# Optimization experiments

Hardware: AMD Instinct MI355X
Metric: run time of the kernel (lower is better)

The kernel has to match this reference:

```python
import jax, jax.numpy as jnp
import numpy as np

D_MODEL = 1024
D_STATE = 16
D_CONV = 3
EXPAND = 2
D_INNER = EXPAND * D_MODEL
BATCH = 1
SEQ = 2048


def _xavier(key, fan_in, fan_out, shape):
    lim = float(np.sqrt(6.0 / (fan_in + fan_out)))
    return jax.random.uniform(key, shape, jnp.float32, -lim, lim)


def setup_inputs() -> dict:
    key = jax.random.key(0)
    ks = jax.random.split(key, 8)
    return {
        "x": jax.random.normal(ks[0], (BATCH, SEQ, D_MODEL), jnp.float32),
        # torch Linear weight (out,in) stored transposed as (in,out) for x @ W
        "in_proj_w": _xavier(ks[1], D_MODEL, 2 * D_INNER, (D_MODEL, 2 * D_INNER)),
        "in_proj_b": jnp.zeros((2 * D_INNER,), jnp.float32),
        "conv_w": _xavier(ks[2], D_MODEL * D_CONV, D_INNER, (D_INNER, D_MODEL, D_CONV)),
        "conv_b": jax.random.normal(ks[3], (D_INNER,), jnp.float32) * 0.02,
        # A_log shifted negative so softplus(A_log) is tiny and the (unstable-by-construction)
        # recurrence with A_bar=exp(+A*dt)>1 stays finite over SEQ steps
        "A_log": jax.random.normal(ks[4], (D_INNER, D_STATE), jnp.float32) * 0.1 - 6.0,
        "D": jnp.ones((D_INNER,), jnp.float32),
        "x_proj_w": _xavier(ks[5], D_INNER, 2 * D_STATE, (D_INNER, 2 * D_STATE)),
        "x_proj_b": jnp.zeros((2 * D_STATE,), jnp.float32),
        "gate_w": _xavier(ks[6], D_INNER, D_INNER, (D_INNER, D_INNER)),
        "gate_b": jnp.zeros((D_INNER,), jnp.float32),
        "o_proj_w": _xavier(ks[7], D_INNER, D_MODEL, (D_INNER, D_MODEL)),
        "o_proj_b": jnp.zeros((D_MODEL,), jnp.float32),
    }


def _forward(x, in_proj_w, in_proj_b, conv_w, conv_b, A_log, D, x_proj_w, x_proj_b,
             gate_w, gate_b, o_proj_w, o_proj_b):
    B, S, _ = x.shape
    # causal depthful conv: torch pads both sides by d_conv-1 then truncates to S,
    # which equals left-pad-only by d_conv-1
    xc = jax.lax.conv_general_dilated(
        x.transpose(0, 2, 1), conv_w, (1,), [(D_CONV - 1, 0)],
        dimension_numbers=("NCH", "OIH", "NCH"))
    x_conv = xc.transpose(0, 2, 1) + conv_b            # (B,S,d_inner)

    xz = x @ in_proj_w + in_proj_b                      # (B,S,2*d_inner)
    z = xz[..., D_INNER:]                               # gate branch (x_inner unused)

    A = jax.nn.softplus(A_log)                          # (d_inner,d_state)
    bc = x_conv @ x_proj_w + x_proj_b                   # (B,S,2*d_state)
    Bm, Cm = bc[..., :D_STATE], bc[..., D_STATE:]
    dt = jax.nn.sigmoid(jnp.mean(x_conv, axis=-1, keepdims=True)) + 0.001  # (B,S,1)
    gate = jax.nn.sigmoid(x_conv @ gate_w + gate_b)
    u = x_conv * gate                                   # (B,S,d_inner)

    dtE = dt[..., None]                                 # (B,S,1,1)
    A_bar = jnp.exp(A[None, None] * dtE)                # (B,S,d_inner,d_state)
    B_bar = A_bar * Bm[:, :, None, :] * dtE             # (B,S,d_inner,d_state)

    def step(h, inp):
        ab, bb, ut, ct = inp                            # (B,di,ds),(B,di,ds),(B,di),(B,ds)
        h = ab * h + bb * ut[:, :, None]
        y = jnp.einsum("bds,bs->bd", h, ct) + D * ut
        return h, y

    h0 = jnp.zeros((B, D_INNER, D_STATE), x.dtype)
    _, ys = jax.lax.scan(
        step, h0,
        (A_bar.transpose(1, 0, 2, 3), B_bar.transpose(1, 0, 2, 3),
         u.transpose(1, 0, 2), Cm.transpose(1, 0, 2)))
    out = ys.transpose(1, 0, 2) * jax.nn.sigmoid(z)     # (B,S,d_inner)
    return out @ o_proj_w + o_proj_b                    # (B,S,d_model)


def reference(x, in_proj_w, in_proj_b, conv_w, conv_b, A_log, D, x_proj_w, x_proj_b,
              gate_w, gate_b, o_proj_w, o_proj_b):
    return _forward(x, in_proj_w, in_proj_b, conv_w, conv_b, A_log, D,
                    x_proj_w, x_proj_b, gate_w, gate_b, o_proj_w, o_proj_b)
```

## Files before the change

kernel.cpp:

```cpp
#include <hip/hip_runtime.h>
#include <hip/hip_bf16.h>
#include <math.h>

typedef __attribute__((ext_vector_type(8))) short short8;
typedef __attribute__((ext_vector_type(4))) float f32x4;

#define NCH 128
#define CT 16

__device__ __forceinline__ unsigned short f2bf(float f) {
  unsigned u = __builtin_bit_cast(unsigned, f);
  u += 0x7fffu + ((u >> 16) & 1u);
  return (unsigned short)(u >> 16);
}
__device__ __forceinline__ float bf2f(unsigned short u) {
  return __builtin_bit_cast(float, (unsigned)u << 16);
}
__device__ __forceinline__ float sigm(float x) { return 1.f / (1.f + __expf(-x)); }

__device__ __forceinline__ void stage16(const void* g, void* l) {
  __builtin_amdgcn_global_load_lds(
      (const __attribute__((address_space(1))) unsigned int*)(unsigned long long)g,
      (__attribute__((address_space(3))) unsigned int*)(unsigned)(unsigned long long)l,
      16, 0, 0);
}

__global__ void prep_xpad(const float* __restrict__ x, unsigned short* __restrict__ xb) {
  int idx = (blockIdx.x * 256 + threadIdx.x) * 4;
  if (idx >= 2050 * 1024) return;
  int row = idx >> 10, col = idx & 1023;
  float v0 = 0.f, v1 = 0.f, v2 = 0.f, v3 = 0.f;
  if (row >= 2) {
    const float4 v = *(const float4*)(x + (size_t)(row - 2) * 1024 + col);
    v0 = v.x; v1 = v.y; v2 = v.z; v3 = v.w;
  }
  unsigned long long pk = (unsigned long long)f2bf(v0)
      | ((unsigned long long)f2bf(v1) << 16)
      | ((unsigned long long)f2bf(v2) << 32)
      | ((unsigned long long)f2bf(v3) << 48);
  *(unsigned long long*)(xb + idx) = pk;
}

__global__ void prep_convw(const float* __restrict__ cw, unsigned short* __restrict__ cwt) {
  int idx = blockIdx.x * 256 + threadIdx.x;
  int d = idx >> 10, i = idx & 1023;
  const float* p = cw + (size_t)d * 3072 + (size_t)i * 3;
  unsigned short* q = cwt + (size_t)d * 3072 + i;
  q[0] = f2bf(p[0]);
  q[1024] = f2bf(p[1]);
  q[2048] = f2bf(p[2]);
}

__global__ void prep_cA(const float* __restrict__ A_log, float* __restrict__ cAb) {
  int i = blockIdx.x * 256 + threadIdx.x;
  cAb[i] = log1pf(__expf(A_log[i]));
}

__global__ void transpose_bf16(const float* __restrict__ W, int src_ld, int col_off,
                               unsigned short* __restrict__ Wt, int rowsI) {
  __shared__ float tile[32][33];
  int n0 = blockIdx.x * 32, i0 = blockIdx.y * 32;
  int tx = threadIdx.x & 31, ty = threadIdx.x >> 5;
#pragma unroll
  for (int rr = 0; rr < 32; rr += 8)
    tile[ty + rr][tx] = W[(size_t)(i0 + ty + rr) * src_ld + col_off + n0 + tx];
  __syncthreads();
#pragma unroll
  for (int rr = 0; rr < 32; rr += 8)
    Wt[(size_t)(n0 + ty + rr) * rowsI + i0 + tx] = f2bf(tile[tx][ty + rr]);
}

template <int MODE, int BM, int BN>
__global__ __launch_bounds__(256, 2) void gemm_t(
    const unsigned short* __restrict__ A, int lda,
    const unsigned short* __restrict__ Bt, int ldb, int K,
    const float* __restrict__ bias,
    float* __restrict__ outf, int ldo,
    unsigned short* __restrict__ outb,
    const unsigned short* __restrict__ mulsrc) {
  constexpr int MR = BM / 32;
  constexpr int NR = BN / 32;
  constexpr int IA = BM / 32;
  constexpr int IB = BN / 32;
  constexpr int L = IA + IB;
  __shared__ unsigned short As[3][BM * 64];
  __shared__ unsigned short Bs[3][BN * 64];

  const int tid = threadIdx.x;
  const int lane = tid & 63;
  const int w = tid >> 6;
  const int wr = w >> 1, wc = w & 1;
  const int bm = blockIdx.x, bn = blockIdx.y;

  f32x4 acc[MR][NR];
#pragma unroll
  for (int m = 0; m < MR; ++m)
#pragma unroll
    for (int n = 0; n < NR; ++n)
#pragma unroll
      for (int j = 0; j < 4; ++j) acc[m][n][j] = 0.f;

  const int srow = lane >> 3;
  const int sslot = (lane & 7) ^ srow;
  const unsigned short* Ab = A + (size_t)(bm * BM + srow) * lda + sslot * 8;
  const unsigned short* Bb = Bt + (size_t)(bn * BN + srow) * ldb + sslot * 8;

  const int r = lane & 15;
  const int g = lane >> 4;
  const int nk = K >> 6;

  auto stage = [&](int buf, int k0) {
#pragma unroll
    for (int i = 0; i < IA; ++i) {
      const int cb = w * IA + i;
      stage16(Ab + (size_t)(cb * 8) * lda + k0, &As[buf][cb * 512]);
    }
#pragma unroll
    for (int i = 0; i < IB; ++i) {
      const int cb = w * IB + i;
      stage16(Bb + (size_t)(cb * 8) * ldb + k0, &Bs[buf][cb * 512]);
    }
  };

  auto compute = [&](int buf) {
#pragma unroll
    for (int kk = 0; kk < 64; kk += 32) {
      const int sb = (kk >> 3) + g;
      short8 af[MR], bfr[NR];
#pragma unroll
      for (int m = 0; m < MR; ++m) {
        const int R = wr * (BM / 2) + m * 16 + r;
        af[m] = *(const short8*)&As[buf][R * 64 + ((sb ^ (R & 7)) << 3)];
      }
#pragma unroll
      for (int n = 0; n < NR; ++n) {
        const int R = wc * (BN / 2) + n * 16 + r;
        bfr[n] = *(const short8*)&Bs[buf][R * 64 + ((sb ^ (R & 7)) << 3)];
      }
#pragma unroll
      for (int m = 0; m < MR; ++m)
#pragma unroll
        for (int n = 0; n < NR; ++n)
          acc[m][n] = __builtin_amdgcn_mfma_f32_16x16x32_bf16(af[m], bfr[n], acc[m][n], 0, 0, 0);
    }
  };

  stage(0, 0);
  stage(1, 64);
  int cur = 0, nxt = 2;
  for (int kt = 0; kt < nk; ++kt) {
    if (kt + 2 < nk) {
      stage(nxt, (kt + 2) * 64);
      asm volatile("s_waitcnt vmcnt(%c0)" ::"i"(2 * L) : "memory");
    } else if (kt + 1 < nk) {
      asm volatile("s_waitcnt vmcnt(%c0)" ::"i"(L) : "memory");
    } else {
      asm volatile("s_waitcnt vmcnt(0)" ::: "memory");
    }
    __builtin_amdgcn_s_barrier();
    __builtin_amdgcn_sched_barrier(0);
    compute(cur);
    __builtin_amdgcn_s_barrier();
    cur = (cur == 2) ? 0 : cur + 1;
    nxt = (nxt == 2) ? 0 : nxt + 1;
  }

  const int cc = lane & 15;
  const int cr = g * 4;
#pragma unroll
  for (int m = 0; m < MR; ++m) {
#pragma unroll
    for (int n = 0; n < NR; ++n) {
      const int col = bn * BN + wc * (BN / 2) + n * 16 + cc;
      const float bv = bias[col];
#pragma unroll
      for (int j = 0; j < 4; ++j) {
        const int row = bm * BM + wr * (BM / 2) + m * 16 + cr + j;
        const size_t o = (size_t)row * ldo + col;
        float v = acc[m][n][j] + bv;
        if (MODE == 0) { outb[o] = f2bf(v); }
        else if (MODE == 1) { outf[o] = v; }
        else { outb[o] = f2bf(bf2f(mulsrc[o]) * sigm(v)); }
      }
    }
  }
}

#define RB 4
__global__ __launch_bounds__(256) void bcdt(const unsigned short* __restrict__ xcb,
                                            const float* __restrict__ xpw,
                                            const float* __restrict__ xpb,
                                            float* __restrict__ Bc, float* __restrict__ Cc,
                                            float* __restrict__ dt) {
  int s0 = blockIdx.x * RB;
  __shared__ float row[RB][2048];
  __shared__ float pj[RB][8][32];
  const int lane = threadIdx.x & 63, wv = threadIdx.x >> 6;
  for (int i = threadIdx.x; i < RB * 256; i += 256) {
    int ri = i >> 8, c8 = i & 255;
    short8 v = *(const short8*)&xcb[(size_t)(s0 + ri) * 2048 + c8 * 8];
#pragma unroll
    for (int j = 0; j < 8; ++j) row[ri][c8 * 8 + j] = bf2f((unsigned short)v[j]);
  }
  __syncthreads();
  {
    float l = 0.f;
    for (int i = lane; i < 2048; i += 64) l += row[wv][i];
#pragma unroll
    for (int off = 32; off > 0; off >>= 1) l += __shfl_down(l, off);
    if (lane == 0) dt[s0 + wv] = sigm(l * (1.f / 2048.f)) + 0.001f;
  }
  const int j = threadIdx.x & 31, seg = threadIdx.x >> 5;
  float acc[RB] = {0.f, 0.f, 0.f, 0.f};
  const int kbase = seg * 256;
  for (int k = 0; k < 256; ++k) {
    float wv2 = xpw[(size_t)(kbase + k) * 32 + j];
#pragma unroll
    for (int ri = 0; ri < RB; ++ri) acc[ri] += row[ri][kbase + k] * wv2;
  }
#pragma unroll
  for (int ri = 0; ri < RB; ++ri) pj[ri][seg][j] = acc[ri];
  __syncthreads();
  if (threadIdx.x < 32 * RB) {
    int ri = threadIdx.x >> 5, jj = threadIdx.x & 31;
    float v = xpb[jj];
#pragma unroll
    for (int q = 0; q < 8; ++q) v += pj[ri][q][jj];
    if (jj < 16) Bc[(size_t)(s0 + ri) * 16 + jj] = v;
    else Cc[(size_t)(s0 + ri) * 16 + jj - 16] = v;
  }
}

__global__ void dtcum(const float* __restrict__ dt, float* __restrict__ T,
                      float* __restrict__ S) {
  int c = threadIdx.x;
  if (c < NCH) {
    float acc = 0.f;
#pragma unroll
    for (int t = 0; t < CT; ++t) {
      acc += dt[c * CT + t];
      T[c * CT + t] = acc;
    }
    S[c] = acc;
  }
}

__global__ __launch_bounds__(256) void scan_local(const float* __restrict__ cAb,
                                                  const float* __restrict__ dt,
                                                  const float* __restrict__ Bc,
                                                  const float* __restrict__ Cc,
                                                  const unsigned short* __restrict__ u,
                                                  const float* __restrict__ Dp,
                                                  unsigned short* __restrict__ yloc,
                                                  float* __restrict__ Hend) {
  const int d0 = blockIdx.x * 256;
  const int d = d0 + threadIdx.x;
  const int c = blockIdx.y;
  __shared__ float sU[CT][256];
  __shared__ float sB[CT][16], sC[CT][16], sdt[CT];
  for (int i = threadIdx.x; i < CT * 32; i += 256) {
    int t = i >> 5, c8 = i & 31;
    short8 v = *(const short8*)&u[(size_t)(c * CT + t) * 2048 + d0 + c8 * 8];
#pragma unroll
    for (int j = 0; j < 8; ++j) sU[t][c8 * 8 + j] = bf2f((unsigned short)v[j]);
  }
  for (int i = threadIdx.x; i < CT * 16; i += 256) {
    sB[i >> 4][i & 15] = Bc[(size_t)c * CT * 16 + i];
    sC[i >> 4][i & 15] = Cc[(size_t)c * CT * 16 + i];
  }
  if (threadIdx.x < CT) sdt[threadIdx.x] = dt[c * CT + threadIdx.x];
  __syncthreads();
  float cA[16], h[16];
#pragma unroll
  for (int n = 0; n < 16; ++n) {
    cA[n] = cAb[(size_t)d * 16 + n];
    h[n] = 0.f;
  }
  const float Dv = Dp[d];
  for (int t = 0; t < CT; ++t) {
    const float dtv = sdt[t];
    const float uv = sU[t][threadIdx.x];
    const float du = dtv * uv;
    float y = Dv * uv;
#pragma unroll
    for (int n = 0; n < 16; ++n) {
      float ab = __expf(cA[n] * dtv);
      h[n] = ab * (h[n] + sB[t][n] * du);
      y += h[n] * sC[t][n];
    }
    yloc[(size_t)(c * CT + t) * 2048 + d] = f2bf(y);
  }
#pragma unroll
  for (int n = 0; n < 16; ++n) Hend[(size_t)c * 32768 + (size_t)d * 16 + n] = h[n];
}

__global__ __launch_bounds__(64) void scan_carry(const float* __restrict__ cAb,
                                                 const float* __restrict__ S,
                                                 float* H) {
  const int g = blockIdx.x * 64 + threadIdx.x;
  const float cA = cAb[g];
  __shared__ float sS[NCH];
  for (int i = threadIdx.x; i < NCH; i += 64) sS[i] = S[i];
  __syncthreads();
  float h = 0.f;
  for (int cb = 0; cb < NCH; cb += 16) {
    float hl[16];
#pragma unroll
    for (int i = 0; i < 16; ++i) hl[i] = H[(size_t)(cb + i) * 32768 + g];
#pragma unroll
    for (int i = 0; i < 16; ++i) {
      H[(size_t)(cb + i) * 32768 + g] = h;
      h = __expf(cA * sS[cb + i]) * h + hl[i];
    }
  }
}

__global__ __launch_bounds__(256) void scan_final(const float* __restrict__ cAb,
                                                  const float* __restrict__ T,
                                                  const float* __restrict__ Cc,
                                                  const unsigned short* __restrict__ yloc,
                                                  const unsigned short* __restrict__ zpre,
                                                  const float* __restrict__ H,
                                                  unsigned short* __restrict__ ob) {
  const int d = blockIdx.x * 256 + threadIdx.x;
  const int c = blockIdx.y;
  __shared__ float sC[CT][16], sT[CT];
  for (int i = threadIdx.x; i < CT * 16; i += 256) sC[i >> 4][i & 15] = Cc[(size_t)c * CT * 16 + i];
  if (threadIdx.x < CT) sT[threadIdx.x] = T[c * CT + threadIdx.x];
  __syncthreads();
  float cA[16], h0[16];
#pragma unroll
  for (int n = 0; n < 16; ++n) {
    cA[n] = cAb[(size_t)d * 16 + n];
    h0[n] = H[(size_t)c * 32768 + (size_t)d * 16 + n];
  }
  for (int t = 0; t < CT; ++t) {
    const size_t idx = (size_t)(c * CT + t) * 2048 + d;
    const float Tt = sT[t];
    float y = bf2f(yloc[idx]);
#pragma unroll
    for (int n = 0; n < 16; ++n) y += sC[t][n] * __expf(cA[n] * Tt) * h0[n];
    ob[idx] = f2bf(y * sigm(bf2f(zpre[idx])));
  }
}

extern "C" void kernel_launch(void* const* d_in, const int* in_sizes, int n_in,
                              void* d_out, int out_size, void* d_ws, size_t ws_size,
                              hipStream_t stream) {
  (void)in_sizes; (void)n_in; (void)out_size; (void)ws_size;
  const float* x = (const float*)d_in[0];
  const float* in_proj_w = (const float*)d_in[1];
  const float* in_proj_b = (const float*)d_in[2];
  const float* conv_w = (const float*)d_in[3];
  const float* conv_b = (const float*)d_in[4];
  const float* A_log = (const float*)d_in[5];
  const float* Dp = (const float*)d_in[6];
  const float* x_proj_w = (const float*)d_in[7];
  const float* x_proj_b = (const float*)d_in[8];
  const float* gate_w = (const float*)d_in[9];
  const float* gate_b = (const float*)d_in[10];
  const float* o_proj_w = (const float*)d_in[11];
  const float* o_proj_b = (const float*)d_in[12];

  char* ws = (char*)d_ws;
  size_t off = 0;
  unsigned short* xb = (unsigned short*)(ws + off); off += (size_t)2050 * 1024 * 2;
  off = (off + 255) & ~(size_t)255;
  unsigned short* cwt = (unsigned short*)(ws + off); off += (size_t)2048 * 3072 * 2;
  unsigned short* wzt = (unsigned short*)(ws + off); off += (size_t)2048 * 1024 * 2;
  unsigned short* gwt = (unsigned short*)(ws + off); off += (size_t)2048 * 2048 * 2;
  unsigned short* owt = (unsigned short*)(ws + off); off += (size_t)1024 * 2048 * 2;
  unsigned short* xcb = (unsigned short*)(ws + off); off += (size_t)2048 * 2048 * 2;
  unsigned short* zpre_b = (unsigned short*)(ws + off); off += (size_t)2048 * 2048 * 2;
  unsigned short* uu_b = (unsigned short*)(ws + off); off += (size_t)2048 * 2048 * 2;
  unsigned short* yloc = (unsigned short*)(ws + off); off += (size_t)2048 * 2048 * 2;
  float* dtv = (float*)(ws + off); off += (size_t)2048 * 4;
  float* Bc = (float*)(ws + off); off += (size_t)2048 * 16 * 4;
  float* Cc = (float*)(ws + off); off += (size_t)2048 * 16 * 4;
  float* Tcum = (float*)(ws + off); off += (size_t)2048 * 4;
  float* Ssum = (float*)(ws + off); off += (size_t)NCH * 4;
  float* cAb = (float*)(ws + off); off += (size_t)32768 * 4;
  float* H = (float*)(ws + off); off += (size_t)NCH * 32768 * 4;
  unsigned short* ob = xcb;

  prep_xpad<<<2050, 256, 0, stream>>>(x, xb);
  prep_convw<<<8192, 256, 0, stream>>>(conv_w, cwt);
  prep_cA<<<128, 256, 0, stream>>>(A_log, cAb);
  transpose_bf16<<<dim3(64, 32), 256, 0, stream>>>(in_proj_w, 4096, 2048, wzt, 1024);
  transpose_bf16<<<dim3(64, 64), 256, 0, stream>>>(gate_w, 2048, 0, gwt, 2048);
  transpose_bf16<<<dim3(32, 64), 256, 0, stream>>>(o_proj_w, 1024, 0, owt, 2048);

  gemm_t<0, 128, 64><<<dim3(16, 32), 256, 0, stream>>>(xb, 1024, cwt, 3072, 3072, conv_b, nullptr, 2048, xcb, nullptr);
  gemm_t<0, 128, 64><<<dim3(16, 32), 256, 0, stream>>>(xb + 2 * 1024, 1024, wzt, 1024, 1024, in_proj_b + 2048, nullptr, 2048, zpre_b, nullptr);
  bcdt<<<512, 256, 0, stream>>>(xcb, x_proj_w, x_proj_b, Bc, Cc, dtv);
  dtcum<<<1, 128, 0, stream>>>(dtv, Tcum, Ssum);
  gemm_t<2, 128, 64><<<dim3(16, 32), 256, 0, stream>>>(xcb, 2048, gwt, 2048, 2048, gate_b, nullptr, 2048, uu_b, xcb);

  scan_local<<<dim3(8, NCH), 256, 0, stream>>>(cAb, dtv, Bc, Cc, uu_b, Dp, yloc, H);
  scan_carry<<<512, 64, 0, stream>>>(cAb, Ssum, H);
  scan_final<<<dim3(8, NCH), 256, 0, stream>>>(cAb, Tcum, Cc, yloc, zpre_b, H, ob);

  gemm_t<1, 64, 64><<<dim3(32, 16), 256, 0, stream>>>(ob, 2048, owt, 2048, 2048, o_proj_b, (float*)d_out, 1024, nullptr, nullptr);
}
```

Measured before the change: 178.9 us.

## Merge prep kernels, fuse conv and z GEMMs, fold dtcum into scans

Six preprocessing kernels are merged into one launch that dispatches on block index. The conv and z-projection GEMMs are merged into one launch using 128x128 tiles with double buffering, and the gate GEMM also moves to 128x128 tiles. The separate dtcum kernel is removed: chunk sums are computed inside scan_carry and prefix sums inside scan_final. The aim is fewer launches and less per-launch overhead, at the cost of fewer blocks per GEMM and a shallower prefetch pipeline.

```diff
diff --git a/kernel.cpp b/kernel.cpp
--- a/kernel.cpp
+++ b/kernel.cpp
@@ -25,41 +25,64 @@
       16, 0, 0);
 }
 
-__global__ void prep_xpad(const float* __restrict__ x, unsigned short* __restrict__ xb) {
-  int idx = (blockIdx.x * 256 + threadIdx.x) * 4;
-  if (idx >= 2050 * 1024) return;
-  int row = idx >> 10, col = idx & 1023;
-  float v0 = 0.f, v1 = 0.f, v2 = 0.f, v3 = 0.f;
-  if (row >= 2) {
-    const float4 v = *(const float4*)(x + (size_t)(row - 2) * 1024 + col);
-    v0 = v.x; v1 = v.y; v2 = v.z; v3 = v.w;
-  }
-  unsigned long long pk = (unsigned long long)f2bf(v0)
-      | ((unsigned long long)f2bf(v1) << 16)
-      | ((unsigned long long)f2bf(v2) << 32)
-      | ((unsigned long long)f2bf(v3) << 48);
-  *(unsigned long long*)(xb + idx) = pk;
-}
-
-__global__ void prep_convw(const float* __restrict__ cw, unsigned short* __restrict__ cwt) {
-  int idx = blockIdx.x * 256 + threadIdx.x;
-  int d = idx >> 10, i = idx & 1023;
-  const float* p = cw + (size_t)d * 3072 + (size_t)i * 3;
-  unsigned short* q = cwt + (size_t)d * 3072 + i;
-  q[0] = f2bf(p[0]);
-  q[1024] = f2bf(p[1]);
-  q[2048] = f2bf(p[2]);
-}
-
-__global__ void prep_cA(const float* __restrict__ A_log, float* __restrict__ cAb) {
-  int i = blockIdx.x * 256 + threadIdx.x;
-  cAb[i] = log1pf(__expf(A_log[i]));
-}
-
-__global__ void transpose_bf16(const float* __restrict__ W, int src_ld, int col_off,
-                               unsigned short* __restrict__ Wt, int rowsI) {
+__global__ __launch_bounds__(256) void prep_uber(
+    const float* __restrict__ x, const float* __restrict__ conv_w,
+    const float* __restrict__ A_log, const float* __restrict__ in_proj_w,
+    const float* __restrict__ gate_w, const float* __restrict__ o_proj_w,
+    unsigned short* __restrict__ xb, unsigned short* __restrict__ cwt,
+    float* __restrict__ cAb, unsigned short* __restrict__ wzt,
+    unsigned short* __restrict__ gwt, unsigned short* __restrict__ owt) {
   __shared__ float tile[32][33];
-  int n0 = blockIdx.x * 32, i0 = blockIdx.y * 32;
+  int bx = blockIdx.x;
+  if (bx < 2050) {
+    int idx = (bx * 256 + threadIdx.x) * 4;
+    if (idx >= 2050 * 1024) return;
+    int row = idx >> 10, col = idx & 1023;
+    float v0 = 0.f, v1 = 0.f, v2 = 0.f, v3 = 0.f;
+    if (row >= 2) {
+      const float4 v = *(const float4*)(x + (size_t)(row - 2) * 1024 + col);
+      v0 = v.x; v1 = v.y; v2 = v.z; v3 = v.w;
+    }
+    unsigned long long pk = (unsigned long long)f2bf(v0)
+        | ((unsigned long long)f2bf(v1) << 16)
+        | ((unsigned long long)f2bf(v2) << 32)
+        | ((unsigned long long)f2bf(v3) << 48);
+    *(unsigned long long*)(xb + idx) = pk;
+    return;
+  }
+  bx -= 2050;
+  if (bx < 8192) {
+    int idx = bx * 256 + threadIdx.x;
+    int d = idx >> 10, i = idx & 1023;
+    const float* p = conv_w + (size_t)d * 3072 + (size_t)i * 3;
+    unsigned short* q = cwt + (size_t)d * 3072 + i;
+    q[0] = f2bf(p[0]);
+    q[1024] = f2bf(p[1]);
+    q[2048] = f2bf(p[2]);
+    return;
+  }
+  bx -= 8192;
+  if (bx < 128) {
+    int i = bx * 256 + threadIdx.x;
+    cAb[i] = log1pf(__expf(A_log[i]));
+    return;
+  }
+  bx -= 128;
+  const float* W;
+  unsigned short* Wt;
+  int src_ld, col_off, rowsI, n0, i0;
+  if (bx < 2048) {
+    W = in_proj_w; Wt = wzt; src_ld = 4096; col_off = 2048; rowsI = 1024;
+    n0 = (bx & 63) * 32; i0 = (bx >> 6) * 32;
+  } else if (bx < 2048 + 4096) {
+    int b = bx - 2048;
+    W = gate_w; Wt = gwt; src_ld = 2048; col_off = 0; rowsI = 2048;
+    n0 = (b & 63) * 32; i0 = (b >> 6) * 32;
+  } else {
+    int b = bx - 2048 - 4096;
+    W = o_proj_w; Wt = owt; src_ld = 1024; col_off = 0; rowsI = 2048;
+    n0 = (b & 31) * 32; i0 = (b >> 5) * 32;
+  }
   int tx = threadIdx.x & 31, ty = threadIdx.x >> 5;
 #pragma unroll
   for (int rr = 0; rr < 32; rr += 8)
@@ -70,77 +93,197 @@
     Wt[(size_t)(n0 + ty + rr) * rowsI + i0 + tx] = f2bf(tile[tx][ty + rr]);
 }
 
-template <int MODE, int BM, int BN>
-__global__ __launch_bounds__(256, 2) void gemm_t(
+template <int MODE>
+__device__ __forceinline__ void gemm_sq_body(
     const unsigned short* __restrict__ A, int lda,
     const unsigned short* __restrict__ Bt, int ldb, int K,
     const float* __restrict__ bias,
     float* __restrict__ outf, int ldo,
     unsigned short* __restrict__ outb,
-    const unsigned short* __restrict__ mulsrc) {
-  constexpr int MR = BM / 32;
-  constexpr int NR = BN / 32;
-  constexpr int IA = BM / 32;
-  constexpr int IB = BN / 32;
-  constexpr int L = IA + IB;
-  __shared__ unsigned short As[3][BM * 64];
-  __shared__ unsigned short Bs[3][BN * 64];
-
+    const unsigned short* __restrict__ mulsrc,
+    int bm, int bn,
+    unsigned short (*As)[128 * 64], unsigned short (*Bs)[128 * 64]) {
+  const int tid = threadIdx.x;
+  const int lane = tid & 63;
+  const int w = tid >> 6;
+  const int wr = w >> 1, wc = w & 1;
+
+  f32x4 acc[4][4];
+#pragma unroll
+  for (int m = 0; m < 4; ++m)
+#pragma unroll
+    for (int n = 0; n < 4; ++n)
+#pragma unroll
+      for (int j = 0; j < 4; ++j) acc[m][n][j] = 0.f;
+
+  const int srow = lane >> 3;
+  const int sslot = (lane & 7) ^ srow;
+  const unsigned short* Ab = A + (size_t)(bm * 128 + srow) * lda + sslot * 8;
+  const unsigned short* Bb = Bt + (size_t)(bn * 128 + srow) * ldb + sslot * 8;
+
+  const int r = lane & 15;
+  const int g = lane >> 4;
+  const int nk = K >> 6;
+
+  auto stage = [&](int buf, int k0) {
+#pragma unroll
+    for (int i = 0; i < 4; ++i) {
+      const int cb = w * 4 + i;
+      stage16(Ab + (size_t)(cb * 8) * lda + k0, &As[buf][cb * 512]);
+    }
+#pragma unroll
+    for (int i = 0; i < 4; ++i) {
+      const int cb = w * 4 + i;
+      stage16(Bb + (size_t)(cb * 8) * ldb + k0, &Bs[buf][cb * 512]);
+    }
+  };
+
+  auto compute = [&](int buf) {
+#pragma unroll
+    for (int kk = 0; kk < 64; kk += 32) {
+      const int sb = (kk >> 3) + g;
+      short8 af[4], bfr[4];
+#pragma unroll
+      for (int m = 0; m < 4; ++m) {
+        const int R = wr * 64 + m * 16 + r;
+        af[m] = *(const short8*)&As[buf][R * 64 + ((sb ^ (R & 7)) << 3)];
+      }
+#pragma unroll
+      for (int n = 0; n < 4; ++n) {
+        const int R = wc * 64 + n * 16 + r;
+        bfr[n] = *(const short8*)&Bs[buf][R * 64 + ((sb ^ (R & 7)) << 3)];
+      }
+#pragma unroll
+      for (int m = 0; m < 4; ++m)
+#pragma unroll
+        for (int n = 0; n < 4; ++n)
+          acc[m][n] = __builtin_amdgcn_mfma_f32_16x16x32_bf16(af[m], bfr[n], acc[m][n], 0, 0, 0);
+    }
+  };
+
+  stage(0, 0);
+  int cur = 0;
+  for (int kt = 0; kt < nk; ++kt) {
+    if (kt + 1 < nk) {
+      stage(cur ^ 1, (kt + 1) * 64);
+      asm volatile("s_waitcnt vmcnt(8)" ::: "memory");
+    } else {
+      asm volatile("s_waitcnt vmcnt(0)" ::: "memory");
+    }
+    __builtin_amdgcn_s_barrier();
+    __builtin_amdgcn_sched_barrier(0);
+    compute(cur);
+    __builtin_amdgcn_s_barrier();
+    cur ^= 1;
+  }
+
+  const int cc = lane & 15;
+  const int cr = g * 4;
+#pragma unroll
+  for (int m = 0; m < 4; ++m) {
+#pragma unroll
+    for (int n = 0; n < 4; ++n) {
+      const int col = bn * 128 + wc * 64 + n * 16 + cc;
+      const float bv = bias[col];
+#pragma unroll
+      for (int j = 0; j < 4; ++j) {
+        const int row = bm * 128 + wr * 64 + m * 16 + cr + j;
+        const size_t o = (size_t)row * ldo + col;
+        float v = acc[m][n][j] + bv;
+        if (MODE == 0) { outb[o] = f2bf(v); }
+        else if (MODE == 1) { outf[o] = v; }
+        else { outb[o] = f2bf(bf2f(mulsrc[o]) * sigm(v)); }
+      }
+    }
+  }
+}
+
+__global__ __launch_bounds__(256, 2) void gemm_convz(
+    const unsigned short* __restrict__ xb,
+    const unsigned short* __restrict__ cwt,
+    const unsigned short* __restrict__ wzt,
+    const float* __restrict__ conv_b,
+    const float* __restrict__ z_b,
+    unsigned short* __restrict__ xcb,
+    unsigned short* __restrict__ zpre_b) {
+  __shared__ unsigned short As[2][128 * 64];
+  __shared__ unsigned short Bs[2][128 * 64];
+  const bool isz = blockIdx.y >= 16;
+  gemm_sq_body<0>(isz ? xb + 2048 : xb, 1024,
+                  isz ? wzt : cwt, isz ? 1024 : 3072, isz ? 1024 : 3072,
+                  isz ? z_b : conv_b, nullptr, 2048,
+                  isz ? zpre_b : xcb, nullptr,
+                  blockIdx.x, isz ? blockIdx.y - 16 : blockIdx.y, As, Bs);
+}
+
+__global__ __launch_bounds__(256, 2) void gemm_gate(
+    const unsigned short* __restrict__ xcb,
+    const unsigned short* __restrict__ gwt,
+    const float* __restrict__ gate_b,
+    unsigned short* __restrict__ uu_b) {
+  __shared__ unsigned short As[2][128 * 64];
+  __shared__ unsigned short Bs[2][128 * 64];
+  gemm_sq_body<2>(xcb, 2048, gwt, 2048, 2048, gate_b, nullptr, 2048, uu_b, xcb,
+                  blockIdx.x, blockIdx.y, As, Bs);
+}
+
+__global__ __launch_bounds__(256, 2) void gemm_out(
+    const unsigned short* __restrict__ A, int lda,
+    const unsigned short* __restrict__ Bt, int ldb, int K,
+    const float* __restrict__ bias,
+    float* __restrict__ outf, int ldo) {
+  constexpr int L = 4;
+  __shared__ unsigned short As[3][64 * 64];
+  __shared__ unsigned short Bs[3][64 * 64];
   const int tid = threadIdx.x;
   const int lane = tid & 63;
   const int w = tid >> 6;
   const int wr = w >> 1, wc = w & 1;
   const int bm = blockIdx.x, bn = blockIdx.y;
 
-  f32x4 acc[MR][NR];
-#pragma unroll
-  for (int m = 0; m < MR; ++m)
-#pragma unroll
-    for (int n = 0; n < NR; ++n)
+  f32x4 acc[2][2];
+#pragma unroll
+  for (int m = 0; m < 2; ++m)
+#pragma unroll
+    for (int n = 0; n < 2; ++n)
 #pragma unroll
       for (int j = 0; j < 4; ++j) acc[m][n][j] = 0.f;
 
   const int srow = lane >> 3;
   const int sslot = (lane & 7) ^ srow;
-  const unsigned short* Ab = A + (size_t)(bm * BM + srow) * lda + sslot * 8;
-  const unsigned short* Bb = Bt + (size_t)(bn * BN + srow) * ldb + sslot * 8;
-
+  const unsigned short* Ab = A + (size_t)(bm * 64 + srow) * lda + sslot * 8;
+  const unsigned short* Bb = Bt + (size_t)(bn * 64 + srow) * ldb + sslot * 8;
   const int r = lane & 15;
   const int g = lane >> 4;
   const int nk = K >> 6;
 
   auto stage = [&](int buf, int k0) {
 #pragma unroll
-    for (int i = 0; i < IA; ++i) {
-      const int cb = w * IA + i;
+    for (int i = 0; i < 2; ++i) {
+      const int cb = w * 2 + i;
       stage16(Ab + (size_t)(cb * 8) * lda + k0, &As[buf][cb * 512]);
-    }
-#pragma unroll
-    for (int i = 0; i < IB; ++i) {
-      const int cb = w * IB + i;
       stage16(Bb + (size_t)(cb * 8) * ldb + k0, &Bs[buf][cb * 512]);
     }
   };
-
   auto compute = [&](int buf) {
 #pragma unroll
     for (int kk = 0; kk < 64; kk += 32) {
       const int sb = (kk >> 3) + g;
-      short8 af[MR], bfr[NR];
-#pragma unroll
-      for (int m = 0; m < MR; ++m) {
-        const int R = wr * (BM / 2) + m * 16 + r;
+      short8 af[2], bfr[2];
+#pragma unroll
+      for (int m = 0; m < 2; ++m) {
+        const int R = wr * 32 + m * 16 + r;
         af[m] = *(const short8*)&As[buf][R * 64 + ((sb ^ (R & 7)) << 3)];
       }
 #pragma unroll
-      for (int n = 0; n < NR; ++n) {
-        const int R = wc * (BN / 2) + n * 16 + r;
+      for (int n = 0; n < 2; ++n) {
+        const int R = wc * 32 + n * 16 + r;
         bfr[n] = *(const short8*)&Bs[buf][R * 64 + ((sb ^ (R & 7)) << 3)];
       }
 #pragma unroll
-      for (int m = 0; m < MR; ++m)
-#pragma unroll
-        for (int n = 0; n < NR; ++n)
+      for (int m = 0; m < 2; ++m)
+#pragma unroll
+        for (int n = 0; n < 2; ++n)
           acc[m][n] = __builtin_amdgcn_mfma_f32_16x16x32_bf16(af[m], bfr[n], acc[m][n], 0, 0, 0);
     }
   };
@@ -168,22 +311,17 @@
   const int cc = lane & 15;
   const int cr = g * 4;
 #pragma unroll
-  for (int m = 0; m < MR; ++m) {
-#pragma unroll
-    for (int n = 0; n < NR; ++n) {
-      const int col = bn * BN + wc * (BN / 2) + n * 16 + cc;
+  for (int m = 0; m < 2; ++m)
+#pragma unroll
+    for (int n = 0; n < 2; ++n) {
+      const int col = bn * 64 + wc * 32 + n * 16 + cc;
       const float bv = bias[col];
 #pragma unroll
       for (int j = 0; j < 4; ++j) {
-        const int row = bm * BM + wr * (BM / 2) + m * 16 + cr + j;
-        const size_t o = (size_t)row * ldo + col;
-        float v = acc[m][n][j] + bv;
-        if (MODE == 0) { outb[o] = f2bf(v); }
-        else if (MODE == 1) { outf[o] = v; }
-        else { outb[o] = f2bf(bf2f(mulsrc[o]) * sigm(v)); }
+        const int row = bm * 64 + wr * 32 + m * 16 + cr + j;
+        outf[(size_t)row * ldo + col] = acc[m][n][j] + bv;
       }
     }
-  }
 }
 
 #define RB 4
@@ -228,20 +366,6 @@
     for (int q = 0; q < 8; ++q) v += pj[ri][q][jj];
     if (jj < 16) Bc[(size_t)(s0 + ri) * 16 + jj] = v;
     else Cc[(size_t)(s0 + ri) * 16 + jj - 16] = v;
-  }
-}
-
-__global__ void dtcum(const float* __restrict__ dt, float* __restrict__ T,
-                      float* __restrict__ S) {
-  int c = threadIdx.x;
-  if (c < NCH) {
-    float acc = 0.f;
-#pragma unroll
-    for (int t = 0; t < CT; ++t) {
-      acc += dt[c * CT + t];
-      T[c * CT + t] = acc;
-    }
-    S[c] = acc;
   }
 }
 
@@ -294,14 +418,22 @@
   for (int n = 0; n < 16; ++n) Hend[(size_t)c * 32768 + (size_t)d * 16 + n] = h[n];
 }
 
-__global__ __launch_bounds__(64) void scan_carry(const float* __restrict__ cAb,
-                                                 const float* __restrict__ S,
-                                                 float* H) {
-  const int g = blockIdx.x * 64 + threadIdx.x;
+__global__ __launch_bounds__(256) void scan_carry(const float* __restrict__ cAb,
+                                                  const float* __restrict__ dt,
+                                                  float* H) {
+  const int g = blockIdx.x * 256 + threadIdx.x;
+  __shared__ float sdt[2048];
+  __shared__ float sS[NCH];
+  for (int i = threadIdx.x; i < 2048; i += 256) sdt[i] = dt[i];
+  __syncthreads();
+  if (threadIdx.x < NCH) {
+    float s = 0.f;
+#pragma unroll
+    for (int t = 0; t < CT; ++t) s += sdt[threadIdx.x * CT + t];
+    sS[threadIdx.x] = s;
+  }
+  __syncthreads();
   const float cA = cAb[g];
-  __shared__ float sS[NCH];
-  for (int i = threadIdx.x; i < NCH; i += 64) sS[i] = S[i];
-  __syncthreads();
   float h = 0.f;
   for (int cb = 0; cb < NCH; cb += 16) {
     float hl[16];
@@ -316,7 +448,7 @@
 }
 
 __global__ __launch_bounds__(256) void scan_final(const float* __restrict__ cAb,
-                                                  const float* __restrict__ T,
+                                                  const float* __restrict__ dt,
                                                   const float* __restrict__ Cc,
                                                   const unsigned short* __restrict__ yloc,
                                                   const unsigned short* __restrict__ zpre,
@@ -324,9 +456,15 @@
                                                   unsigned short* __restrict__ ob) {
   const int d = blockIdx.x * 256 + threadIdx.x;
   const int c = blockIdx.y;
-  __shared__ float sC[CT][16], sT[CT];
+  __shared__ float sC[CT][16], sT[CT], sdt[CT];
   for (int i = threadIdx.x; i < CT * 16; i += 256) sC[i >> 4][i & 15] = Cc[(size_t)c * CT * 16 + i];
-  if (threadIdx.x < CT) sT[threadIdx.x] = T[c * CT + threadIdx.x];
+  if (threadIdx.x < CT) sdt[threadIdx.x] = dt[c * CT + threadIdx.x];
+  __syncthreads();
+  if (threadIdx.x < CT) {
+    float a = 0.f;
+    for (int t = 0; t <= threadIdx.x; ++t) a += sdt[t];
+    sT[threadIdx.x] = a;
+  }
   __syncthreads();
   float cA[16], h0[16];
 #pragma unroll
@@ -377,28 +515,20 @@
   float* dtv = (float*)(ws + off); off += (size_t)2048 * 4;
   float* Bc = (float*)(ws + off); off += (size_t)2048 * 16 * 4;
   float* Cc = (float*)(ws + off); off += (size_t)2048 * 16 * 4;
-  float* Tcum = (float*)(ws + off); off += (size_t)2048 * 4;
-  float* Ssum = (float*)(ws + off); off += (size_t)NCH * 4;
   float* cAb = (float*)(ws + off); off += (size_t)32768 * 4;
   float* H = (float*)(ws + off); off += (size_t)NCH * 32768 * 4;
   unsigned short* ob = xcb;
 
-  prep_xpad<<<2050, 256, 0, stream>>>(x, xb);
-  prep_convw<<<8192, 256, 0, stream>>>(conv_w, cwt);
-  prep_cA<<<128, 256, 0, stream>>>(A_log, cAb);
-  transpose_bf16<<<dim3(64, 32), 256, 0, stream>>>(in_proj_w, 4096, 2048, wzt, 1024);
-  transpose_bf16<<<dim3(64, 64), 256, 0, stream>>>(gate_w, 2048, 0, gwt, 2048);
-  transpose_bf16<<<dim3(32, 64), 256, 0, stream>>>(o_proj_w, 1024, 0, owt, 2048);
-
-  gemm_t<0, 128, 64><<<dim3(16, 32), 256, 0, stream>>>(xb, 1024, cwt, 3072, 3072, conv_b, nullptr, 2048, xcb, nullptr);
-  gemm_t<0, 128, 64><<<dim3(16, 32), 256, 0, stream>>>(xb + 2 * 1024, 1024, wzt, 1024, 1024, in_proj_b + 2048, nullptr, 2048, zpre_b, nullptr);
+  prep_uber<<<18562, 256, 0, stream>>>(x, conv_w, A_log, in_proj_w, gate_w, o_proj_w,
+                                       xb, cwt, cAb, wzt, gwt, owt);
+
+  gemm_convz<<<dim3(16, 32), 256, 0, stream>>>(xb, cwt, wzt, conv_b, in_proj_b + 2048, xcb, zpre_b);
   bcdt<<<512, 256, 0, stream>>>(xcb, x_proj_w, x_proj_b, Bc, Cc, dtv);
-  dtcum<<<1, 128, 0, stream>>>(dtv, Tcum, Ssum);
-  gemm_t<2, 128, 64><<<dim3(16, 32), 256, 0, stream>>>(xcb, 2048, gwt, 2048, 2048, gate_b, nullptr, 2048, uu_b, xcb);
+  gemm_gate<<<dim3(16, 16), 256, 0, stream>>>(xcb, gwt, gate_b, uu_b);
 
   scan_local<<<dim3(8, NCH), 256, 0, stream>>>(cAb, dtv, Bc, Cc, uu_b, Dp, yloc, H);
-  scan_carry<<<512, 64, 0, stream>>>(cAb, Ssum, H);
-  scan_final<<<dim3(8, NCH), 256, 0, stream>>>(cAb, Tcum, Cc, yloc, zpre_b, H, ob);
-
-  gemm_t<1, 64, 64><<<dim3(32, 16), 256, 0, stream>>>(ob, 2048, owt, 2048, 2048, o_proj_b, (float*)d_out, 1024, nullptr, nullptr);
-}
+  scan_carry<<<128, 256, 0, stream>>>(cAb, dtv, H);
+  scan_final<<<dim3(8, NCH), 256, 0, stream>>>(cAb, dtv, Cc, yloc, zpre_b, H, ob);
+
+  gemm_out<<<dim3(32, 16), 256, 0, stream>>>(ob, 2048, owt, 2048, 2048, o_proj_b, (float*)d_out, 1024);
+}
```

Result: faster. 157.3 us (-12.1%).
